# Performance work log

Hardware: AMD Instinct MI355X
Metric: run time of the kernel (lower is better)

## Reference

```python
import jax, jax.numpy as jnp
import numpy as np

B, IN, OUT, K, TOPK = 1024, 4096, 4096, 64, 64


def setup_inputs() -> dict:
    key = jax.random.key(0)
    k0, k1, k2, k3 = jax.random.split(key, 4)
    return {
        "x": jax.random.normal(k0, (B, K), dtype=jnp.float32),
        "weight": jax.random.normal(k1, (OUT, IN), dtype=jnp.float32) / np.float32(np.sqrt(IN)),
        "bias": jax.random.normal(k2, (OUT,), dtype=jnp.float32) * 0.01,
        "prev_idx": jax.random.randint(k3, (B, K), 0, IN),
        "top_k": TOPK,
    }


def reference(x, weight, bias, prev_idx, top_k):
    # Per-sample column gather of the weight matrix: (OUT, B, K)
    gathered = jnp.take(weight, prev_idx, axis=1)
    # Batched matvec (torch.bmm with input.unsqueeze(-1)) + bias -> (B, OUT)
    result = jnp.einsum('obk,bk->bo', gathered, x) + bias
    # top-k select; torch.gather(result, 1, topk_indices) == top-k values
    vals, sel = jax.lax.top_k(result, top_k)
    return vals, sel
```

## Files before the change

kernel.cpp:

```cpp
#include <hip/hip_runtime.h>
#include <stdint.h>
#include <math.h>


#define NB    1024
#define NIN   4096
#define NOUT  4096
#define NK    64
#define NTOPK 64
#define OTILE 4

__global__ __launch_bounds__(256) void pack_kernel(const float* __restrict__ x,
                                                   const int* __restrict__ idx,
                                                   float* __restrict__ xt,
                                                   int* __restrict__ idxt) {
    int tid = blockIdx.x * 256 + threadIdx.x;
    int k = tid >> 10;
    int b = tid & 1023;
    idxt[tid] = idx[(b << 6) + k];
    xt[tid]   = x[(b << 6) + k];
}

__global__ __launch_bounds__(512) void gemm_kernel(const float* __restrict__ xt,
                                                   const int* __restrict__ idxt,
                                                   const float* __restrict__ W,
                                                   const float* __restrict__ bias,
                                                   double* __restrict__ C) {
    __shared__ float Wt[NIN * OTILE];
    const int t  = threadIdx.x;
    const int o0 = blockIdx.x * OTILE;

    for (int r = 0; r < OTILE; ++r) {
        const float4* src = reinterpret_cast<const float4*>(W + (size_t)(o0 + r) * NIN);
        for (int j = t; j < NIN / 4; j += 512) {
            float4 v = src[j];
            int i = j << 2;
            Wt[(i + 0) * OTILE + r] = v.x;
            Wt[(i + 1) * OTILE + r] = v.y;
            Wt[(i + 2) * OTILE + r] = v.z;
            Wt[(i + 3) * OTILE + r] = v.w;
        }
    }
    __syncthreads();

    double acc[2][OTILE];
    for (int r = 0; r < OTILE; ++r) {
        double bd = (double)bias[o0 + r];
        acc[0][r] = bd;
        acc[1][r] = bd;
    }

    const int b0 = t << 1;
    const int*   ip = idxt + b0;
    const float* xp = xt + b0;

#pragma unroll 4
    for (int k = 0; k < NK; ++k) {
        const int2   iv = *reinterpret_cast<const int2*>(ip + (k << 10));
        const float2 xv = *reinterpret_cast<const float2*>(xp + (k << 10));
        const float4 w0 = *reinterpret_cast<const float4*>(Wt + iv.x * OTILE);
        const float4 w1 = *reinterpret_cast<const float4*>(Wt + iv.y * OTILE);
        double x0 = (double)xv.x, x1 = (double)xv.y;
        acc[0][0] += x0 * (double)w0.x; acc[0][1] += x0 * (double)w0.y;
        acc[0][2] += x0 * (double)w0.z; acc[0][3] += x0 * (double)w0.w;
        acc[1][0] += x1 * (double)w1.x; acc[1][1] += x1 * (double)w1.y;
        acc[1][2] += x1 * (double)w1.z; acc[1][3] += x1 * (double)w1.w;
    }

    for (int c = 0; c < 2; ++c) {
        double* dst = C + (size_t)(b0 + c) * NOUT + o0;
        dst[0] = acc[c][0]; dst[1] = acc[c][1];
        dst[2] = acc[c][2]; dst[3] = acc[c][3];
    }
}

__device__ inline unsigned keyf(double d) {
    unsigned u = __float_as_uint((float)d);
    return (u & 0x80000000u) ? ~u : (u | 0x80000000u);
}

__global__ __launch_bounds__(256) void topk_kernel(const double* __restrict__ C,
                                                   float* __restrict__ outv,
                                                   float* __restrict__ outi) {
    __shared__ unsigned hist[4096];
    __shared__ double   cval[1024];
    __shared__ int      cidx[1024];
    __shared__ unsigned part[256];
    __shared__ int      sBstar;
    __shared__ unsigned sCnt;

    const int t = threadIdx.x;
    const int b = blockIdx.x;
    const double* row = C + (size_t)b * NOUT;

    for (int j = t; j < 4096; j += 256) hist[j] = 0u;
    if (t == 0) sCnt = 0u;
    __syncthreads();

    for (int j = t; j < NOUT; j += 256)
        atomicAdd(&hist[keyf(row[j]) >> 20], 1u);
    __syncthreads();

    {
        unsigned s = 0;
        for (int q = 0; q < 16; ++q) s += hist[t * 16 + q];
        part[t] = s;
    }
    __syncthreads();
    for (int off = 1; off < 256; off <<= 1) {
        unsigned v = (t + off < 256) ? part[t + off] : 0u;
        __syncthreads();
        part[t] += v;
        __syncthreads();
    }
    {
        unsigned run = (t < 255) ? part[t + 1] : 0u;
        for (int q = 15; q >= 0; --q) {
            int bin = t * 16 + q;
            unsigned cge = run + hist[bin];
            if (cge >= 64u && run < 64u) sBstar = bin;
            run = cge;
        }
    }
    __syncthreads();

    const unsigned Bstar = (unsigned)sBstar;
    for (int j = t; j < NOUT; j += 256) {
        double v = row[j];
        if ((keyf(v) >> 20) >= Bstar) {
            unsigned pos = atomicAdd(&sCnt, 1u);
            if (pos < 1024u) { cval[pos] = v; cidx[pos] = j; }
        }
    }
    __syncthreads();

    int M = (int)sCnt; if (M > 1024) M = 1024;
    int n = 64; while (n < M) n <<= 1;
    for (int j = M + t; j < n; j += 256) { cval[j] = -INFINITY; cidx[j] = 0x7fffffff; }
    __syncthreads();

    for (int kk = 2; kk <= n; kk <<= 1) {
        for (int jj = kk >> 1; jj > 0; jj >>= 1) {
            for (int i = t; i < n; i += 256) {
                int l = i ^ jj;
                if (l > i) {
                    double v1 = cval[i], v2 = cval[l];
                    int    i1 = cidx[i], i2 = cidx[l];
                    bool first = (v1 > v2) || (v1 == v2 && i1 < i2);
                    bool asc   = ((i & kk) == 0);
                    if (first != asc) {
                        cval[i] = v2; cval[l] = v1;
                        cidx[i] = i2; cidx[l] = i1;
                    }
                }
            }
            __syncthreads();
        }
    }

    if (t < 64) {
        outv[(b << 6) + t] = (float)cval[t];
        outi[(b << 6) + t] = (float)cidx[t];
    }
}

extern "C" void kernel_launch(void* const* d_in, const int* in_sizes, int n_in,
                              void* d_out, int out_size, void* d_ws, size_t ws_size,
                              hipStream_t stream) {
    const float* x    = (const float*)d_in[0];
    const float* W    = (const float*)d_in[1];
    const float* bias = (const float*)d_in[2];
    const int*   idx  = (const int*)d_in[3];

    char*   ws   = (char*)d_ws;
    double* C    = (double*)ws;
    int*    idxt = (int*)(ws + (size_t)NB * NOUT * sizeof(double));
    float*  xt   = (float*)(ws + (size_t)NB * NOUT * sizeof(double)
                               + (size_t)NB * NK * sizeof(int));

    float* outv = (float*)d_out;
    float* outi = outv + NB * NTOPK;

    pack_kernel<<<(NB * NK) / 256, 256, 0, stream>>>(x, idx, xt, idxt);
    gemm_kernel<<<NOUT / OTILE, 512, 0, stream>>>(xt, idxt, W, bias, C);
    topk_kernel<<<NB, 256, 0, stream>>>(C, outv, outi);
}
```

Baseline: 174.5 us.

## Fuse index/x packing, swizzle LDS weight tile, register-cache top-k rows

```diff
diff --git a/kernel.cpp b/kernel.cpp
--- a/kernel.cpp
+++ b/kernel.cpp
@@ -8,59 +8,63 @@
 #define NOUT  4096
 #define NK    64
 #define NTOPK 64
-#define OTILE 4
+
+__device__ __forceinline__ int SWZ(int i) { return i ^ ((i >> 3) & 7); }
 
 __global__ __launch_bounds__(256) void pack_kernel(const float* __restrict__ x,
                                                    const int* __restrict__ idx,
-                                                   float* __restrict__ xt,
-                                                   int* __restrict__ idxt) {
+                                                   int2* __restrict__ fused) {
     int tid = blockIdx.x * 256 + threadIdx.x;
     int k = tid >> 10;
     int b = tid & 1023;
-    idxt[tid] = idx[(b << 6) + k];
-    xt[tid]   = x[(b << 6) + k];
-}
-
-__global__ __launch_bounds__(512) void gemm_kernel(const float* __restrict__ xt,
-                                                   const int* __restrict__ idxt,
+    int   iv = idx[(b << 6) + k];
+    float xv = x[(b << 6) + k];
+    fused[tid] = make_int2(SWZ(iv) << 4, __float_as_int(xv));
+}
+
+__global__ __launch_bounds__(512) void gemm_kernel(const int2* __restrict__ fused,
                                                    const float* __restrict__ W,
                                                    const float* __restrict__ bias,
                                                    double* __restrict__ C) {
-    __shared__ float Wt[NIN * OTILE];
+    __shared__ float4 Wt[NIN];
     const int t  = threadIdx.x;
-    const int o0 = blockIdx.x * OTILE;
-
-    for (int r = 0; r < OTILE; ++r) {
-        const float4* src = reinterpret_cast<const float4*>(W + (size_t)(o0 + r) * NIN);
-        for (int j = t; j < NIN / 4; j += 512) {
-            float4 v = src[j];
-            int i = j << 2;
-            Wt[(i + 0) * OTILE + r] = v.x;
-            Wt[(i + 1) * OTILE + r] = v.y;
-            Wt[(i + 2) * OTILE + r] = v.z;
-            Wt[(i + 3) * OTILE + r] = v.w;
-        }
-    }
-    __syncthreads();
-
-    double acc[2][OTILE];
-    for (int r = 0; r < OTILE; ++r) {
+    const int o0 = blockIdx.x * 4;
+
+    const float4* w0p = reinterpret_cast<const float4*>(W + (size_t)(o0 + 0) * NIN);
+    const float4* w1p = reinterpret_cast<const float4*>(W + (size_t)(o0 + 1) * NIN);
+    const float4* w2p = reinterpret_cast<const float4*>(W + (size_t)(o0 + 2) * NIN);
+    const float4* w3p = reinterpret_cast<const float4*>(W + (size_t)(o0 + 3) * NIN);
+#pragma unroll
+    for (int m = 0; m < 2; ++m) {
+        int j = t + m * 512;
+        float4 r0 = w0p[j], r1 = w1p[j], r2 = w2p[j], r3 = w3p[j];
+        int i0 = j << 2;
+        Wt[SWZ(i0 + 0)] = make_float4(r0.x, r1.x, r2.x, r3.x);
+        Wt[SWZ(i0 + 1)] = make_float4(r0.y, r1.y, r2.y, r3.y);
+        Wt[SWZ(i0 + 2)] = make_float4(r0.z, r1.z, r2.z, r3.z);
+        Wt[SWZ(i0 + 3)] = make_float4(r0.w, r1.w, r2.w, r3.w);
+    }
+    __syncthreads();
+
+    double acc[2][4];
+    for (int r = 0; r < 4; ++r) {
         double bd = (double)bias[o0 + r];
         acc[0][r] = bd;
         acc[1][r] = bd;
     }
 
     const int b0 = t << 1;
-    const int*   ip = idxt + b0;
-    const float* xp = xt + b0;
+    const int4* fp = reinterpret_cast<const int4*>(fused + b0);
 
 #pragma unroll 4
     for (int k = 0; k < NK; ++k) {
-        const int2   iv = *reinterpret_cast<const int2*>(ip + (k << 10));
-        const float2 xv = *reinterpret_cast<const float2*>(xp + (k << 10));
-        const float4 w0 = *reinterpret_cast<const float4*>(Wt + iv.x * OTILE);
-        const float4 w1 = *reinterpret_cast<const float4*>(Wt + iv.y * OTILE);
-        double x0 = (double)xv.x, x1 = (double)xv.y;
+        int4 f = fp[k * 512];
+        const float4 w0 = *reinterpret_cast<const float4*>(
+            reinterpret_cast<const char*>(Wt) + f.x);
+        const float4 w1 = *reinterpret_cast<const float4*>(
+            reinterpret_cast<const char*>(Wt) + f.z);
+        double x0 = (double)__int_as_float(f.y);
+        double x1 = (double)__int_as_float(f.w);
         acc[0][0] += x0 * (double)w0.x; acc[0][1] += x0 * (double)w0.y;
         acc[0][2] += x0 * (double)w0.z; acc[0][3] += x0 * (double)w0.w;
         acc[1][0] += x1 * (double)w1.x; acc[1][1] += x1 * (double)w1.y;
@@ -74,7 +78,7 @@
     }
 }
 
-__device__ inline unsigned keyf(double d) {
+__device__ __forceinline__ unsigned keyf(double d) {
     unsigned u = __float_as_uint((float)d);
     return (u & 0x80000000u) ? ~u : (u | 0x80000000u);
 }
@@ -90,15 +94,19 @@
     __shared__ unsigned sCnt;
 
     const int t = threadIdx.x;
-    const int b = blockIdx.x;
-    const double* row = C + (size_t)b * NOUT;
+    const double* row = C + (size_t)blockIdx.x * NOUT;
+
+    double v[16];
+#pragma unroll
+    for (int q = 0; q < 16; ++q) v[q] = row[q * 256 + t];
 
     for (int j = t; j < 4096; j += 256) hist[j] = 0u;
     if (t == 0) sCnt = 0u;
     __syncthreads();
 
-    for (int j = t; j < NOUT; j += 256)
-        atomicAdd(&hist[keyf(row[j]) >> 20], 1u);
+#pragma unroll
+    for (int q = 0; q < 16; ++q)
+        atomicAdd(&hist[keyf(v[q]) >> 20], 1u);
     __syncthreads();
 
     {
@@ -107,12 +115,24 @@
         part[t] = s;
     }
     __syncthreads();
-    for (int off = 1; off < 256; off <<= 1) {
-        unsigned v = (t + off < 256) ? part[t + off] : 0u;
-        __syncthreads();
-        part[t] += v;
-        __syncthreads();
-    }
+
+    if (t < 64) {
+        unsigned c0 = part[4 * t + 0], c1 = part[4 * t + 1];
+        unsigned c2 = part[4 * t + 2], c3 = part[4 * t + 3];
+        unsigned s = c0 + c1 + c2 + c3;
+        unsigned suf = s;
+        for (int off = 1; off < 64; off <<= 1) {
+            unsigned xx = __shfl_down(suf, off);
+            if (t + off < 64) suf += xx;
+        }
+        unsigned below = suf - s;
+        part[4 * t + 3] = below + c3;
+        part[4 * t + 2] = below + c3 + c2;
+        part[4 * t + 1] = below + c3 + c2 + c1;
+        part[4 * t + 0] = below + s;
+    }
+    __syncthreads();
+
     {
         unsigned run = (t < 255) ? part[t + 1] : 0u;
         for (int q = 15; q >= 0; --q) {
@@ -125,11 +145,11 @@
     __syncthreads();
 
     const unsigned Bstar = (unsigned)sBstar;
-    for (int j = t; j < NOUT; j += 256) {
-        double v = row[j];
-        if ((keyf(v) >> 20) >= Bstar) {
+#pragma unroll
+    for (int q = 0; q < 16; ++q) {
+        if ((keyf(v[q]) >> 20) >= Bstar) {
             unsigned pos = atomicAdd(&sCnt, 1u);
-            if (pos < 1024u) { cval[pos] = v; cidx[pos] = j; }
+            if (pos < 1024u) { cval[pos] = v[q]; cidx[pos] = q * 256 + t; }
         }
     }
     __syncthreads();
@@ -159,8 +179,8 @@
     }
 
     if (t < 64) {
-        outv[(b << 6) + t] = (float)cval[t];
-        outi[(b << 6) + t] = (float)cidx[t];
+        outv[(blockIdx.x << 6) + t] = (float)cval[t];
+        outi[(blockIdx.x << 6) + t] = (float)cidx[t];
     }
 }
 
@@ -172,16 +192,14 @@
     const float* bias = (const float*)d_in[2];
     const int*   idx  = (const int*)d_in[3];
 
-    char*   ws   = (char*)d_ws;
-    double* C    = (double*)ws;
-    int*    idxt = (int*)(ws + (size_t)NB * NOUT * sizeof(double));
-    float*  xt   = (float*)(ws + (size_t)NB * NOUT * sizeof(double)
-                               + (size_t)NB * NK * sizeof(int));
+    char*   ws    = (char*)d_ws;
+    double* C     = (double*)ws;
+    int2*   fused = (int2*)(ws + (size_t)NB * NOUT * sizeof(double));
 
     float* outv = (float*)d_out;
     float* outi = outv + NB * NTOPK;
 
-    pack_kernel<<<(NB * NK) / 256, 256, 0, stream>>>(x, idx, xt, idxt);
-    gemm_kernel<<<NOUT / OTILE, 512, 0, stream>>>(xt, idxt, W, bias, C);
+    pack_kernel<<<(NB * NK) / 256, 256, 0, stream>>>(x, idx, fused);
+    gemm_kernel<<<NOUT / 4, 512, 0, stream>>>(fused, W, bias, C);
     topk_kernel<<<NB, 256, 0, stream>>>(C, outv, outi);
 }
```

Result: faster. 154.2 us (-11.7%).
